# Optimization experiments

Measured on AMD Instinct MI355X. Metric: run time of the kernel, lower is better.

Reference implementation:

```python
import jax, jax.numpy as jnp
import numpy as np

STATE = 1024

def setup_inputs() -> dict:
    key = jax.random.key(0)
    k1, k2, k3, k4, k5 = jax.random.split(key, 5)
    B, IN, S = 4096, 1024, STATE
    stdv = 1.0 / np.sqrt(S)
    return {
        "input": jax.random.normal(k1, (B, IN), jnp.float32),
        "old_h": jax.random.normal(k2, (B, S), jnp.float32),
        "old_cell": jax.random.normal(k3, (B, S), jnp.float32),
        "weights": jax.random.uniform(k4, (4 * S, IN + S), jnp.float32, -stdv, stdv),
        "bias": jax.random.uniform(k5, (4 * S,), jnp.float32, -stdv, stdv),
    }

def reference(input, old_h, old_cell, weights, bias):
    # Fused gate GEMM: X = [input, old_h] -> [B, IN+S]; gates -> [B, 4S]
    X = jnp.concatenate([input, old_h], axis=1)
    gates = X @ weights.T + bias
    f, i, o, g = jnp.split(gates, 4, axis=1)
    f = jax.nn.sigmoid(f)
    i = jax.nn.sigmoid(i)
    o = jax.nn.sigmoid(o)
    g = jnp.tanh(g)
    new_cell = f * old_cell + i * g
    new_h = o * jnp.tanh(new_cell)
    return new_h, new_cell
```

## Files before the change

### kernel.cpp

```cpp
#include <hip/hip_runtime.h>
#include <stdint.h>

#define NB   4096
#define KD   2048
#define ND   4096
#define SD   1024

#define BM   256
#define BN   256
#define BK   64
#define NKT  (KD / BK)

using f32x4  = __attribute__((ext_vector_type(4))) float;
using bf16x8 = __attribute__((ext_vector_type(8))) short;

typedef const __attribute__((address_space(1))) uint32_t* gas_u32;
typedef __attribute__((address_space(3))) uint32_t* las_u32;

__device__ __forceinline__ unsigned short f2bf(float f) {
    union { float f; uint32_t u; } c; c.f = f;
    uint32_t u = c.u;
    uint32_t r = (u + 0x7fffu + ((u >> 16) & 1u)) >> 16;
    return (unsigned short)r;
}

__device__ __forceinline__ void async_load16(const void* gsrc, void* ldst) {
    __builtin_amdgcn_global_load_lds((gas_u32)gsrc, (las_u32)ldst, 16, 0, 0);
}

__device__ __forceinline__ float frcp(float x) { return __builtin_amdgcn_rcpf(x); }
__device__ __forceinline__ float sigm(float x) { return frcp(1.f + __expf(-x)); }
__device__ __forceinline__ float tanh_fast(float x) {
    return 1.f - 2.f * frcp(1.f + __expf(2.f * x));
}

__global__ void pack_kernel(const float* __restrict__ input,
                            const float* __restrict__ old_h,
                            const float* __restrict__ weights,
                            const float* __restrict__ bias,
                            unsigned short* __restrict__ Xb,
                            unsigned short* __restrict__ Wb,
                            float* __restrict__ biasR) {
    const int XCH = NB * (KD / 4);
    const int WCH = ND * (KD / 4);
    const int BCH = ND / 4;
    const int total = XCH + WCH + BCH;
    for (int c = blockIdx.x * blockDim.x + threadIdx.x; c < total;
         c += gridDim.x * blockDim.x) {
        if (c < XCH) {
            int b  = c >> 9;
            int k  = (c & 511) << 2;
            const float* src = (k < 1024) ? (input + (size_t)b * 1024 + k)
                                          : (old_h + (size_t)b * 1024 + (k - 1024));
            float4 v = *reinterpret_cast<const float4*>(src);
            ushort4 o;
            o.x = f2bf(v.x); o.y = f2bf(v.y); o.z = f2bf(v.z); o.w = f2bf(v.w);
            *reinterpret_cast<ushort4*>(Xb + (size_t)b * KD + k) = o;
        } else if (c < XCH + WCH) {
            int cc = c - XCH;
            int n  = cc >> 9;
            int k  = (cc & 511) << 2;
            int srow = ((n >> 4) & 3) * SD + ((n >> 6) * 16 + (n & 15));
            float4 v = *reinterpret_cast<const float4*>(weights + (size_t)srow * KD + k);
            ushort4 o;
            o.x = f2bf(v.x); o.y = f2bf(v.y); o.z = f2bf(v.z); o.w = f2bf(v.w);
            *reinterpret_cast<ushort4*>(Wb + (size_t)n * KD + k) = o;
        } else {
            int n4 = (c - XCH - WCH) << 2;
            #pragma unroll
            for (int t = 0; t < 4; ++t) {
                int n = n4 + t;
                biasR[n] = bias[((n >> 4) & 3) * SD + ((n >> 6) * 16 + (n & 15))];
            }
        }
    }
}

#define SEG(DB, AB, HALF) (((((DB) * 2 + (AB)) * 2) + (HALF)) * 8192)

#define SBAR   __builtin_amdgcn_s_barrier()
#define SFENCE __builtin_amdgcn_sched_barrier(0)
#define ASM_LGKM0  asm volatile("s_waitcnt lgkmcnt(0)" ::: "memory")
#define ASM_VMCNT4 asm volatile("s_waitcnt vmcnt(4)" ::: "memory")

__launch_bounds__(512, 2)
__global__ void lstm_gemm(const unsigned short* __restrict__ Xb,
                          const unsigned short* __restrict__ Wb,
                          const float* __restrict__ biasR,
                          const float* __restrict__ old_cell,
                          float* __restrict__ new_h,
                          float* __restrict__ new_cell) {
    __shared__ unsigned short lds[65536];

    const int tid  = threadIdx.x;
    const int lane = tid & 63;
    const int wid  = tid >> 6;
    const int wm   = wid >> 2;
    const int wn   = wid & 3;
    const int l15  = lane & 15;
    const int krow = lane >> 4;

    const int wg    = blockIdx.x;
    const int swz   = (wg & 7) * 32 + (wg >> 3);
    const int mblk  = swz >> 4;
    const int nblk  = swz & 15;
    const int rbase = mblk * BM;
    const int nbase = nblk * BN;

    const int c0 = tid, c1 = tid + 512;
    const int srow0 = c0 >> 3, sk0 = ((c0 & 7) ^ (srow0 & 7)) * 8;
    const int srow1 = c1 >> 3, sk1 = ((c1 & 7) ^ (srow1 & 7)) * 8;

    f32x4  acc[8][4] = {};
    bf16x8 a[4][2];
    bf16x8 b[2][2][2];

#define STAGE(PTR, TB, KT, DB, AB, HALF) do {                                   \
        async_load16((PTR) + (size_t)((TB) + (HALF) * 128 + srow0) * KD +       \
                         (KT) * BK + sk0,                                       \
                     lds + SEG(DB, AB, HALF) + c0 * 8);                         \
        async_load16((PTR) + (size_t)((TB) + (HALF) * 128 + srow1) * KD +       \
                         (KT) * BK + sk1,                                       \
                     lds + SEG(DB, AB, HALF) + c1 * 8);                         \
    } while (0)

#define LOAD_A(DB, MQ) do {                                                     \
        const unsigned short* base_ = lds + SEG(DB, 0, 0) + wm * 8192;          \
        _Pragma("unroll") for (int i_ = 0; i_ < 4; ++i_)                        \
        _Pragma("unroll") for (int kk_ = 0; kk_ < 2; ++kk_) {                   \
            int r_ = (MQ) * 64 + i_ * 16 + l15;                                 \
            int s_ = kk_ * 4 + krow;                                            \
            a[i_][kk_] = *reinterpret_cast<const bf16x8*>(                      \
                base_ + r_ * 64 + ((s_ ^ (r_ & 7)) * 8));                       \
        }                                                                       \
    } while (0)

#define LOAD_B(DB, NQ) do {                                                     \
        const unsigned short* base_ = lds + SEG(DB, 1, 0) + (wn >> 1) * 8192;   \
        _Pragma("unroll") for (int j_ = 0; j_ < 2; ++j_)                        \
        _Pragma("unroll") for (int kk_ = 0; kk_ < 2; ++kk_) {                   \
            int r_ = (wn & 1) * 64 + ((NQ) * 2 + j_) * 16 + l15;                \
            int s_ = kk_ * 4 + krow;                                            \
            b[NQ][j_][kk_] = *reinterpret_cast<const bf16x8*>(                  \
                base_ + r_ * 64 + ((s_ ^ (r_ & 7)) * 8));                       \
        }                                                                       \
    } while (0)

#define MMA(MQ, NQ) do {                                                        \
        _Pragma("unroll") for (int i_ = 0; i_ < 4; ++i_)                        \
        _Pragma("unroll") for (int j_ = 0; j_ < 2; ++j_)                        \
        _Pragma("unroll") for (int kk_ = 0; kk_ < 2; ++kk_)                     \
            acc[(MQ) * 4 + i_][(NQ) * 2 + j_] =                                 \
                __builtin_amdgcn_mfma_f32_16x16x32_bf16(                        \
                    a[i_][kk_], b[NQ][j_][kk_],                                 \
                    acc[(MQ) * 4 + i_][(NQ) * 2 + j_], 0, 0, 0);                \
    } while (0)

#define PH_HEAD  SFENCE; SBAR; ASM_LGKM0; SFENCE; __builtin_amdgcn_s_setprio(1)
#define PH_TAIL  __builtin_amdgcn_s_setprio(0); SFENCE; SBAR; SFENCE
#define PH_TAILV __builtin_amdgcn_s_setprio(0); SFENCE; ASM_VMCNT4; SBAR; SFENCE

    STAGE(Wb, nbase, 0, 0, 1, 0);
    STAGE(Wb, nbase, 0, 0, 1, 1);
    STAGE(Xb, rbase, 0, 0, 0, 0);
    STAGE(Xb, rbase, 0, 0, 0, 1);
    STAGE(Wb, nbase, 1, 1, 1, 0);
    STAGE(Wb, nbase, 1, 1, 1, 1);
    ASM_VMCNT4;
    SBAR; SFENCE;

    for (int t = 0; t < NKT; t += 2) {
        const int kt1 = t + 1;
        const int kt2 = (t + 2) & (NKT - 1);
        const int kt3 = (t + 3) & (NKT - 1);

        LOAD_A(0, 0); LOAD_B(0, 0); STAGE(Xb, rbase, kt1, 1, 0, 0);
        PH_HEAD; MMA(0, 0); PH_TAIL;
        LOAD_B(0, 1); STAGE(Xb, rbase, kt1, 1, 0, 1);
        PH_HEAD; MMA(0, 1); PH_TAIL;
        LOAD_A(0, 1); STAGE(Wb, nbase, kt2, 0, 1, 0);
        PH_HEAD; MMA(1, 0); PH_TAIL;
        STAGE(Wb, nbase, kt2, 0, 1, 1);
        PH_HEAD; MMA(1, 1); PH_TAILV;

        LOAD_A(1, 0); LOAD_B(1, 0); STAGE(Xb, rbase, kt2, 0, 0, 0);
        PH_HEAD; MMA(0, 0); PH_TAIL;
        LOAD_B(1, 1); STAGE(Xb, rbase, kt2, 0, 0, 1);
        PH_HEAD; MMA(0, 1); PH_TAIL;
        LOAD_A(1, 1); STAGE(Wb, nbase, kt3, 1, 1, 0);
        PH_HEAD; MMA(1, 0); PH_TAIL;
        STAGE(Wb, nbase, kt3, 1, 1, 1);
        PH_HEAD; MMA(1, 1); PH_TAILV;
    }

    const int s = (nblk * 4 + wn) * 16 + l15;
    float bg[4];
    #pragma unroll
    for (int jj = 0; jj < 4; ++jj)
        bg[jj] = biasR[nbase + wn * 64 + jj * 16 + l15];

    #pragma unroll
    for (int mi = 0; mi < 8; ++mi) {
        #pragma unroll
        for (int r = 0; r < 4; ++r) {
            const int row = rbase + wm * 128 + mi * 16 + krow * 4 + r;
            float fg = sigm(acc[mi][0][r] + bg[0]);
            float ig = sigm(acc[mi][1][r] + bg[1]);
            float og = sigm(acc[mi][2][r] + bg[2]);
            float gg = tanh_fast(acc[mi][3][r] + bg[3]);
            float oc = old_cell[(size_t)row * SD + s];
            float nc = fmaf(fg, oc, ig * gg);
            float nh = og * tanh_fast(nc);
            new_h[(size_t)row * SD + s]    = nh;
            new_cell[(size_t)row * SD + s] = nc;
        }
    }
}

extern "C" void kernel_launch(void* const* d_in, const int* in_sizes, int n_in,
                              void* d_out, int out_size, void* d_ws, size_t ws_size,
                              hipStream_t stream) {
    const float* input    = (const float*)d_in[0];
    const float* old_h    = (const float*)d_in[1];
    const float* old_cell = (const float*)d_in[2];
    const float* weights  = (const float*)d_in[3];
    const float* bias     = (const float*)d_in[4];

    unsigned short* Xb  = (unsigned short*)d_ws;
    unsigned short* Wb  = (unsigned short*)((char*)d_ws + (size_t)16777216);
    float*          bR  = (float*)((char*)d_ws + (size_t)33554432);

    float* out_h = (float*)d_out;
    float* out_c = out_h + (size_t)NB * SD;

    pack_kernel<<<2048, 256, 0, stream>>>(input, old_h, weights, bias, Xb, Wb, bR);
    lstm_gemm<<<(NB / BM) * (ND / BN), 512, 0, stream>>>(Xb, Wb, bR, old_cell,
                                                         out_h, out_c);
}
```

Baseline: 80.66 us.

## Overlap LDS fragment loads with MFMA by prefetching next-phase operands

```diff
diff --git a/kernel.cpp b/kernel.cpp
--- a/kernel.cpp
+++ b/kernel.cpp
@@ -81,6 +81,7 @@
 #define SBAR   __builtin_amdgcn_s_barrier()
 #define SFENCE __builtin_amdgcn_sched_barrier(0)
 #define ASM_LGKM0  asm volatile("s_waitcnt lgkmcnt(0)" ::: "memory")
+#define ASM_VMCNT2 asm volatile("s_waitcnt vmcnt(2)" ::: "memory")
 #define ASM_VMCNT4 asm volatile("s_waitcnt vmcnt(4)" ::: "memory")
 
 __launch_bounds__(512, 2)
@@ -113,7 +114,8 @@
 
     f32x4  acc[8][4] = {};
     bf16x8 a[4][2];
-    bf16x8 b[2][2][2];
+    bf16x8 bm[2][2];
+    bf16x8 ba[2][2];
 
 #define STAGE(PTR, TB, KT, DB, AB, HALF) do {                                   \
         async_load16((PTR) + (size_t)((TB) + (HALF) * 128 + srow0) * KD +       \
@@ -135,30 +137,30 @@
         }                                                                       \
     } while (0)
 
-#define LOAD_B(DB, NQ) do {                                                     \
+#define LOAD_B_TO(DST, DB, NQ) do {                                             \
         const unsigned short* base_ = lds + SEG(DB, 1, 0) + (wn >> 1) * 8192;   \
         _Pragma("unroll") for (int j_ = 0; j_ < 2; ++j_)                        \
         _Pragma("unroll") for (int kk_ = 0; kk_ < 2; ++kk_) {                   \
             int r_ = (wn & 1) * 64 + ((NQ) * 2 + j_) * 16 + l15;                \
             int s_ = kk_ * 4 + krow;                                            \
-            b[NQ][j_][kk_] = *reinterpret_cast<const bf16x8*>(                  \
+            DST[j_][kk_] = *reinterpret_cast<const bf16x8*>(                    \
                 base_ + r_ * 64 + ((s_ ^ (r_ & 7)) * 8));                       \
         }                                                                       \
     } while (0)
 
-#define MMA(MQ, NQ) do {                                                        \
+#define MMA_Q(MQ, NQH, BB) do {                                                 \
         _Pragma("unroll") for (int i_ = 0; i_ < 4; ++i_)                        \
         _Pragma("unroll") for (int j_ = 0; j_ < 2; ++j_)                        \
         _Pragma("unroll") for (int kk_ = 0; kk_ < 2; ++kk_)                     \
-            acc[(MQ) * 4 + i_][(NQ) * 2 + j_] =                                 \
+            acc[(MQ) * 4 + i_][(NQH) * 2 + j_] =                                \
                 __builtin_amdgcn_mfma_f32_16x16x32_bf16(                        \
-                    a[i_][kk_], b[NQ][j_][kk_],                                 \
-                    acc[(MQ) * 4 + i_][(NQ) * 2 + j_], 0, 0, 0);                \
-    } while (0)
-
-#define PH_HEAD  SFENCE; SBAR; ASM_LGKM0; SFENCE; __builtin_amdgcn_s_setprio(1)
-#define PH_TAIL  __builtin_amdgcn_s_setprio(0); SFENCE; SBAR; SFENCE
-#define PH_TAILV __builtin_amdgcn_s_setprio(0); SFENCE; ASM_VMCNT4; SBAR; SFENCE
+                    a[i_][kk_], BB[j_][kk_],                                    \
+                    acc[(MQ) * 4 + i_][(NQH) * 2 + j_], 0, 0, 0);               \
+    } while (0)
+
+#define PH_HEAD   SFENCE; SBAR; ASM_LGKM0; SFENCE; __builtin_amdgcn_s_setprio(1)
+#define PH_HEADV  SFENCE; ASM_VMCNT2; SBAR; ASM_LGKM0; SFENCE; __builtin_amdgcn_s_setprio(1)
+#define PH_TAIL   __builtin_amdgcn_s_setprio(0); SFENCE; SBAR; SFENCE
 
     STAGE(Wb, nbase, 0, 0, 1, 0);
     STAGE(Wb, nbase, 0, 0, 1, 1);
@@ -168,29 +170,25 @@
     STAGE(Wb, nbase, 1, 1, 1, 1);
     ASM_VMCNT4;
     SBAR; SFENCE;
+    LOAD_B_TO(bm, 0, 0);
+    LOAD_A(0, 0);
+
+#define KBODY(TT, BUF) do {                                                     \
+        const int kt1_ = ((TT) + 1) & (NKT - 1);                                \
+        const int kt2_ = ((TT) + 2) & (NKT - 1);                                \
+        STAGE(Xb, rbase, kt1_, (BUF) ^ 1, 0, 0);                                \
+        PH_HEAD;  MMA_Q(0, 0, bm); LOAD_B_TO(ba, BUF, 1);      PH_TAIL;         \
+        STAGE(Xb, rbase, kt1_, (BUF) ^ 1, 0, 1);                                \
+        PH_HEAD;  MMA_Q(0, 1, ba); LOAD_A(BUF, 1);             PH_TAIL;         \
+        STAGE(Wb, nbase, kt2_, BUF, 1, 0);                                      \
+        PH_HEADV; MMA_Q(1, 0, bm); LOAD_B_TO(bm, (BUF) ^ 1, 0); PH_TAIL;        \
+        STAGE(Wb, nbase, kt2_, BUF, 1, 1);                                      \
+        PH_HEAD;  MMA_Q(1, 1, ba); LOAD_A((BUF) ^ 1, 0);       PH_TAIL;         \
+    } while (0)
 
     for (int t = 0; t < NKT; t += 2) {
-        const int kt1 = t + 1;
-        const int kt2 = (t + 2) & (NKT - 1);
-        const int kt3 = (t + 3) & (NKT - 1);
-
-        LOAD_A(0, 0); LOAD_B(0, 0); STAGE(Xb, rbase, kt1, 1, 0, 0);
-        PH_HEAD; MMA(0, 0); PH_TAIL;
-        LOAD_B(0, 1); STAGE(Xb, rbase, kt1, 1, 0, 1);
-        PH_HEAD; MMA(0, 1); PH_TAIL;
-        LOAD_A(0, 1); STAGE(Wb, nbase, kt2, 0, 1, 0);
-        PH_HEAD; MMA(1, 0); PH_TAIL;
-        STAGE(Wb, nbase, kt2, 0, 1, 1);
-        PH_HEAD; MMA(1, 1); PH_TAILV;
-
-        LOAD_A(1, 0); LOAD_B(1, 0); STAGE(Xb, rbase, kt2, 0, 0, 0);
-        PH_HEAD; MMA(0, 0); PH_TAIL;
-        LOAD_B(1, 1); STAGE(Xb, rbase, kt2, 0, 0, 1);
-        PH_HEAD; MMA(0, 1); PH_TAIL;
-        LOAD_A(1, 1); STAGE(Wb, nbase, kt3, 1, 1, 0);
-        PH_HEAD; MMA(1, 0); PH_TAIL;
-        STAGE(Wb, nbase, kt3, 1, 1, 1);
-        PH_HEAD; MMA(1, 1); PH_TAILV;
+        KBODY(t, 0);
+        KBODY(t + 1, 1);
     }
 
     const int s = (nblk * 4 + wn) * 16 + l15;
```

Result: faster. 79.02 us (-2.0%).
